# Kernel optimization log

Hardware: AMD Instinct MI355X
Metric: run time of the kernel (lower is better)

Reference implementation:

```python
import jax, jax.numpy as jnp
import numpy as np

N, E, D, G = 50000, 640000, 128, 64
STEPS = 4

def _leaky(z):
    return jnp.where(z >= 0, z, 0.01 * z)

def _lin(x, W, b):
    return x @ W.T + b

def setup_inputs() -> dict:
    key = jax.random.key(0)
    ks = jax.random.split(key, 16)
    s = 0.05
    inp = {
        "x": jax.random.normal(ks[0], (N, D), jnp.float32),
        "x_global": jax.random.normal(ks[1], (G, D), jnp.float32),
        "edge_attr": jax.random.normal(ks[2], (E, 2), jnp.float32),
        # per-step stacked parameters (torch Linear layout [out,in])
        "Wm": jax.random.normal(ks[3], (STEPS, D, D), jnp.float32) * s,
        "bm": jnp.zeros((STEPS, D), jnp.float32),
        "Wa": jax.random.normal(ks[4], (STEPS, D, 2 * D), jnp.float32) * s,
        "ba": jnp.zeros((STEPS, D), jnp.float32),
        "Wgate": jax.random.normal(ks[5], (STEPS, 1, D), jnp.float32) * s,
        "bgate": jnp.zeros((STEPS, 1), jnp.float32),
        "Wfeat": jax.random.normal(ks[6], (STEPS, D, D), jnp.float32) * s,
        "bfeat": jnp.zeros((STEPS, D), jnp.float32),
        "Wt": jax.random.normal(ks[7], (STEPS, D, 2 * D), jnp.float32) * s,
        "bt": jnp.zeros((STEPS, D), jnp.float32),
        "edge_index": jax.random.randint(ks[8], (2, E), 0, N, jnp.int32),
        "batch_ind": jnp.sort(jax.random.randint(ks[9], (N,), 0, G, jnp.int32)),
        "num_graphs": G,
    }
    return inp

def reference(x, x_global, edge_attr, Wm, bm, Wa, ba, Wgate, bgate, Wfeat, bfeat, Wt, bt, edge_index, batch_ind, num_graphs):
    src, dst = edge_index[0], edge_index[1]
    n = x.shape[0]
    for i in range(Wm.shape[0]):
        # GraphNet: gather -> Linear+LeakyReLU -> scatter-max -> concat -> Linear+LeakyReLU + residual
        msg = _leaky(_lin(x[src], Wm[i], bm[i]))                     # [E, agg]
        agg = jax.ops.segment_max(msg, dst, num_segments=n)
        agg = jnp.where(jnp.isfinite(agg), agg, 0.0)                 # PyG fills empty with 0
        x = _leaky(_lin(jnp.concatenate([x, agg], axis=1), Wa[i], ba[i])) + x
        # GlobalNode: attentional aggregation (segment softmax) + transform + residual
        gate = _lin(x, Wgate[i], bgate[i])[:, 0]                     # [N]
        feat = _leaky(_lin(x, Wfeat[i], bfeat[i]))                   # [N, D]
        gmax = jax.ops.segment_max(gate, batch_ind, num_segments=num_graphs)
        gmax = jnp.where(jnp.isfinite(gmax), gmax, 0.0)
        e = jnp.exp(gate - gmax[batch_ind])
        denom = jax.ops.segment_sum(e, batch_ind, num_segments=num_graphs)
        denom = jnp.where(denom == 0, 1.0, denom)
        alpha = e / denom[batch_ind]
        xg = jax.ops.segment_sum(alpha[:, None] * feat, batch_ind, num_segments=num_graphs)
        cat = jnp.concatenate([xg, x_global], axis=1)
        x_global = _leaky(_lin(cat, Wt[i], bt[i])) + x_global
    return (x, x_global)
```

## Files before the change

### kernel.cpp

```cpp
#include <hip/hip_runtime.h>
#include <hip/hip_bf16.h>

#define NN 50000
#define EE 640000
#define DD 128
#define GG 64
#define STEPS 4
#define XP 32
#define NB 196

static inline int cdiv(int a, int b) { return (a + b - 1) / b; }

typedef __attribute__((ext_vector_type(8))) short bf16x8;
typedef __attribute__((ext_vector_type(4))) float f32x4;

__device__ __forceinline__ float lk(float z) { return z >= 0.f ? z : 0.01f * z; }
__device__ __forceinline__ float b2f(short b) { return __uint_as_float(((unsigned)(unsigned short)b) << 16); }
__device__ __forceinline__ unsigned short f2b(float f) {
    unsigned u = __float_as_uint(f);
    return (unsigned short)((u + 0x7FFFu + ((u >> 16) & 1u)) >> 16);
}

__global__ void k_f2b(const float* __restrict__ in, unsigned short* __restrict__ out, int n4) {
    int i = blockIdx.x * blockDim.x + threadIdx.x;
    if (i < n4) {
        float4 v = reinterpret_cast<const float4*>(in)[i];
        ushort4 o;
        o.x = f2b(v.x); o.y = f2b(v.y); o.z = f2b(v.z); o.w = f2b(v.w);
        reinterpret_cast<ushort4*>(out)[i] = o;
    }
}

#define WC1 (STEPS * DD * DD / 4)
#define WC2 (STEPS * DD * 2 * DD / 4)
#define WC3 (STEPS * DD * DD / 4)
__global__ void k_wcvt(const float* __restrict__ Wm, const float* __restrict__ Wa, const float* __restrict__ Wf,
                       unsigned short* __restrict__ Wm_b, unsigned short* __restrict__ Wa_b,
                       unsigned short* __restrict__ Wf_b) {
    int i = blockIdx.x * blockDim.x + threadIdx.x;
    const float* src; unsigned short* dst; int j = i;
    if (j < WC1) { src = Wm; dst = Wm_b; }
    else {
        j -= WC1;
        if (j < WC2) { src = Wa; dst = Wa_b; }
        else {
            j -= WC2;
            if (j >= WC3) return;
            src = Wf; dst = Wf_b;
        }
    }
    float4 v = reinterpret_cast<const float4*>(src)[j];
    ushort4 o;
    o.x = f2b(v.x); o.y = f2b(v.y); o.z = f2b(v.z); o.w = f2b(v.w);
    reinterpret_cast<ushort4*>(dst)[j] = o;
}

__global__ void k_count(const int* __restrict__ dst, int* __restrict__ deg) {
    int e = blockIdx.x * blockDim.x + threadIdx.x;
    if (e < EE) atomicAdd(&deg[dst[e]], 1);
}

__global__ __launch_bounds__(256) void k_scan1(const int* __restrict__ deg, int* __restrict__ off,
                                               int* __restrict__ bsum) {
    __shared__ int ws[4];
    int tid = threadIdx.x, lane = tid & 63, wv = tid >> 6;
    int i = blockIdx.x * 256 + tid;
    int v = (i < NN) ? deg[i] : 0;
    int x = v;
    #pragma unroll
    for (int o = 1; o < 64; o <<= 1) { int t = __shfl_up(x, o); if (lane >= o) x += t; }
    if (lane == 63) ws[wv] = x;
    __syncthreads();
    int wbase = 0;
    #pragma unroll
    for (int p = 0; p < 3; ++p) if (p < wv) wbase += ws[p];
    if (i < NN) off[i] = wbase + x - v;
    if (tid == 255) bsum[blockIdx.x] = wbase + x;
}

__global__ __launch_bounds__(256) void k_scan2(const int* __restrict__ bsum, int* __restrict__ boff,
                                               int* __restrict__ off) {
    __shared__ int ws[4];
    int tid = threadIdx.x, lane = tid & 63, wv = tid >> 6;
    int v = (tid < NB) ? bsum[tid] : 0;
    int x = v;
    #pragma unroll
    for (int o = 1; o < 64; o <<= 1) { int t = __shfl_up(x, o); if (lane >= o) x += t; }
    if (lane == 63) ws[wv] = x;
    __syncthreads();
    int wbase = 0;
    #pragma unroll
    for (int p = 0; p < 3; ++p) if (p < wv) wbase += ws[p];
    if (tid < NB) boff[tid] = wbase + x - v;
    if (tid == 255) off[NN] = wbase + x;
}

__global__ __launch_bounds__(256) void k_scan3(const int* __restrict__ boff, int* __restrict__ off,
                                               int* __restrict__ cursor) {
    int i = blockIdx.x * 256 + threadIdx.x;
    if (i < NN) {
        int o = off[i] + boff[blockIdx.x];
        off[i] = o;
        cursor[i] = o;
    }
}

__global__ void k_fill(const int* __restrict__ src, const int* __restrict__ dst,
                       int* __restrict__ cursor, int* __restrict__ csr) {
    int e = blockIdx.x * blockDim.x + threadIdx.x;
    if (e < EE) {
        int d = dst[e];
        int p = atomicAdd(&cursor[d], 1);
        csr[p] = src[e];
    }
}

__global__ void k_goff(const int* __restrict__ batch, int* __restrict__ goff) {
    int i = blockIdx.x * blockDim.x + threadIdx.x;
    if (i >= NN) return;
    int b = batch[i];
    int prev = (i == 0) ? -1 : batch[i - 1];
    for (int g = prev + 1; g <= b; ++g) goff[g] = i;
    if (i == NN - 1) for (int g = b + 1; g <= GG; ++g) goff[g] = NN;
}

template<int KDIM, bool TWO_IN, bool RESID, bool GATE>
__global__ __launch_bounds__(256) void k_mfma(
    const unsigned short* __restrict__ X1b, const unsigned short* __restrict__ X2b,
    const unsigned short* __restrict__ Wb, const float* __restrict__ bias,
    unsigned short* __restrict__ Yb, float* __restrict__ Yf, const float* __restrict__ resid,
    const float* __restrict__ wgf, const float* __restrict__ bgp, float* __restrict__ gate)
{
    __shared__ float sY[64 * 128];
    const int tid = threadIdx.x;
    const int wv = tid >> 6, lane = tid & 63;
    const int lo = lane & 15, hi = lane >> 4;
    const int n0 = blockIdx.x * 64;
    const int arow = n0 + wv * 16 + lo;
    const bool rvalid = arow < NN;

    f32x4 acc[8];
    #pragma unroll
    for (int t = 0; t < 8; ++t) acc[t] = (f32x4){0.f, 0.f, 0.f, 0.f};

    constexpr int KCH = KDIM / 32;
    #pragma unroll
    for (int kc = 0; kc < KCH; ++kc) {
        const int k = kc * 32 + hi * 8;
        bf16x8 a = (bf16x8)(short)0;
        if (rvalid) {
            if (TWO_IN) {
                const unsigned short* base = (k < 128) ? &X1b[(size_t)arow * 128 + k]
                                                       : &X2b[(size_t)arow * 128 + (k - 128)];
                a = *reinterpret_cast<const bf16x8*>(base);
            } else {
                a = *reinterpret_cast<const bf16x8*>(&X1b[(size_t)arow * KDIM + k]);
            }
        }
        #pragma unroll
        for (int t = 0; t < 8; ++t) {
            const int o = t * 16 + lo;
            bf16x8 b = *reinterpret_cast<const bf16x8*>(&Wb[(size_t)o * KDIM + k]);
            acc[t] = __builtin_amdgcn_mfma_f32_16x16x32_bf16(a, b, acc[t], 0, 0, 0);
        }
    }

    const int lrow = wv * 16 + hi * 4;
    const int swz1 = (hi & 1) << 4;
    #pragma unroll
    for (int t = 0; t < 8; ++t) {
        const int col = (t * 16 + lo) ^ swz1;
        const float bc = bias[t * 16 + lo];
        #pragma unroll
        for (int r = 0; r < 4; ++r)
            sY[(lrow + r) * 128 + col] = lk(acc[t][r] + bc);
    }
    __syncthreads();

    if (RESID) {
        const float bg0 = GATE ? bgp[0] : 0.f;
        #pragma unroll
        for (int it = 0; it < 8; ++it) {
            const int idx = it * 256 + tid;
            const int row = idx >> 5, u4 = (idx & 31) * 4;
            const int n = n0 + row;
            const bool valid = n < NN;
            const int ux = u4 ^ (((row >> 2) & 1) << 4);
            float4 v = *reinterpret_cast<const float4*>(&sY[row * 128 + ux]);
            if (valid) {
                float4 rsd = *reinterpret_cast<const float4*>(&resid[(size_t)n * 128 + u4]);
                v.x += rsd.x; v.y += rsd.y; v.z += rsd.z; v.w += rsd.w;
                *reinterpret_cast<float4*>(&Yf[(size_t)n * 128 + u4]) = v;
                ushort4 ob;
                ob.x = f2b(v.x); ob.y = f2b(v.y); ob.z = f2b(v.z); ob.w = f2b(v.w);
                *reinterpret_cast<ushort4*>(&Yb[(size_t)n * 128 + u4]) = ob;
            }
            if (GATE) {
                float4 wg4 = *reinterpret_cast<const float4*>(&wgf[u4]);
                float gs = valid ? (v.x * wg4.x + v.y * wg4.y + v.z * wg4.z + v.w * wg4.w) : 0.f;
                #pragma unroll
                for (int sh = 16; sh > 0; sh >>= 1) gs += __shfl_xor(gs, sh);
                if ((lane & 31) == 0 && valid) gate[n] = gs + bg0;
            }
        }
    } else {
        #pragma unroll
        for (int it = 0; it < 4; ++it) {
            const int idx = it * 256 + tid;
            const int row = idx >> 4, ub = (idx & 15) * 8;
            const int n = n0 + row;
            if (n < NN) {
                const int ubx = ub ^ (((row >> 2) & 1) << 4);
                bf16x8 ob;
                #pragma unroll
                for (int j = 0; j < 8; ++j) ob[j] = (short)f2b(sY[row * 128 + ubx + j]);
                *reinterpret_cast<bf16x8*>(&Yb[(size_t)n * 128 + ub]) = ob;
            }
        }
    }
}

__global__ __launch_bounds__(256) void k_aggmax(const unsigned short* __restrict__ yb,
                                                const int* __restrict__ off,
                                                const int* __restrict__ csr,
                                                unsigned short* __restrict__ aggb) {
    int gtid = blockIdx.x * blockDim.x + threadIdx.x;
    int node = gtid >> 6;
    if (node >= NN) return;
    int lane = threadIdx.x & 63;
    int slot = lane >> 4, c8 = (lane & 15) * 8;
    int b = off[node], e = off[node + 1];
    int deg = e - b;
    float m[8];
    #pragma unroll
    for (int j = 0; j < 8; ++j) m[j] = -3.4e38f;
    if (deg > 0) {
        int T = (deg + 7) >> 3;
        for (int it = 0; it < T; ++it) {
            int p0 = b + it * 8 + slot;
            int p1 = p0 + 4;
            int i0 = csr[p0 < e ? p0 : b];
            int i1 = csr[p1 < e ? p1 : b];
            bf16x8 v0 = *reinterpret_cast<const bf16x8*>(&yb[(size_t)i0 * 128 + c8]);
            bf16x8 v1 = *reinterpret_cast<const bf16x8*>(&yb[(size_t)i1 * 128 + c8]);
            #pragma unroll
            for (int j = 0; j < 8; ++j) m[j] = fmaxf(m[j], fmaxf(b2f(v0[j]), b2f(v1[j])));
        }
    }
    #pragma unroll
    for (int j = 0; j < 8; ++j) m[j] = fmaxf(m[j], __shfl_xor(m[j], 16));
    #pragma unroll
    for (int j = 0; j < 8; ++j) m[j] = fmaxf(m[j], __shfl_xor(m[j], 32));
    if (slot == 0) {
        bf16x8 o;
        #pragma unroll
        for (int j = 0; j < 8; ++j) o[j] = (deg > 0) ? (short)f2b(m[j]) : (short)0;
        *reinterpret_cast<bf16x8*>(&aggb[(size_t)node * 128 + c8]) = o;
    }
}

__global__ __launch_bounds__(256) void k_gstats(const float* __restrict__ gate, const int* __restrict__ goff,
                                                float* __restrict__ efac, float* __restrict__ invden) {
    __shared__ float red[256];
    int g = blockIdx.x;
    int tid = threadIdx.x;
    int b = goff[g], e = goff[g + 1];
    float m = -3.4e38f;
    for (int i = b + tid; i < e; i += 256) m = fmaxf(m, gate[i]);
    red[tid] = m; __syncthreads();
    for (int o = 128; o > 0; o >>= 1) { if (tid < o) red[tid] = fmaxf(red[tid], red[tid + o]); __syncthreads(); }
    float gm = red[0];
    __syncthreads();
    float s = 0.f;
    for (int i = b + tid; i < e; i += 256) { float ev = __expf(gate[i] - gm); efac[i] = ev; s += ev; }
    red[tid] = s; __syncthreads();
    for (int o = 128; o > 0; o >>= 1) { if (tid < o) red[tid] += red[tid + o]; __syncthreads(); }
    if (tid == 0) { float d = red[0]; if (d == 0.f) d = 1.f; invden[g] = 1.f / d; }
}

__global__ __launch_bounds__(128) void k_xgpart(const float* __restrict__ efac,
                                                const unsigned short* __restrict__ featb,
                                                const int* __restrict__ goff, float* __restrict__ part) {
    int g = blockIdx.x >> 5, p = blockIdx.x & 31;
    int d = threadIdx.x;
    int b = goff[g], e = goff[g + 1];
    int len = e - b;
    int chunk = (len + XP - 1) / XP;
    int s0 = b + p * chunk;
    int s1 = min(e, s0 + chunk);
    float acc = 0.f;
    #pragma unroll 2
    for (int i = s0; i < s1; ++i) acc += efac[i] * b2f(featb[(size_t)i * 128 + d]);
    part[((size_t)g * XP + p) * 128 + d] = acc;
}

__global__ __launch_bounds__(128) void k_gtrans(const float* __restrict__ part, const float* __restrict__ invden,
                                                const float* __restrict__ Wt, const float* __restrict__ bt,
                                                float* __restrict__ xglob) {
    __shared__ float cat[256];
    int g = blockIdx.x;
    int o = threadIdx.x;
    float xgv = 0.f;
    #pragma unroll
    for (int p = 0; p < XP; ++p) xgv += part[((size_t)g * XP + p) * 128 + o];
    cat[o] = xgv * invden[g];
    cat[128 + o] = xglob[(size_t)g * 128 + o];
    __syncthreads();
    float accv = bt[o];
    const float4* w4 = reinterpret_cast<const float4*>(&Wt[(size_t)o * 256]);
    #pragma unroll 8
    for (int k4 = 0; k4 < 64; ++k4) {
        float4 wv = w4[k4];
        accv += cat[4 * k4 + 0] * wv.x + cat[4 * k4 + 1] * wv.y + cat[4 * k4 + 2] * wv.z + cat[4 * k4 + 3] * wv.w;
    }
    float outv = lk(accv) + cat[128 + o];
    xglob[(size_t)g * 128 + o] = outv;
}

extern "C" void kernel_launch(void* const* d_in, const int* in_sizes, int n_in,
                              void* d_out, int out_size, void* d_ws, size_t ws_size,
                              hipStream_t stream) {
    const float* x_in  = (const float*)d_in[0];
    const float* xg_in = (const float*)d_in[1];
    const float* Wm = (const float*)d_in[3];
    const float* bm = (const float*)d_in[4];
    const float* Wa = (const float*)d_in[5];
    const float* ba = (const float*)d_in[6];
    const float* Wg = (const float*)d_in[7];
    const float* bg = (const float*)d_in[8];
    const float* Wf = (const float*)d_in[9];
    const float* bf = (const float*)d_in[10];
    const float* Wt = (const float*)d_in[11];
    const float* bt = (const float*)d_in[12];
    const int* eidx  = (const int*)d_in[13];
    const int* batch = (const int*)d_in[14];

    float* xout  = (float*)d_out;
    float* xglob = xout + (size_t)NN * DD;

    char* w = (char*)d_ws;
    unsigned short* yb   = (unsigned short*)w; w += (size_t)NN * DD * 2;
    unsigned short* aggb = (unsigned short*)w; w += (size_t)NN * DD * 2;
    unsigned short* xb   = (unsigned short*)w; w += (size_t)NN * DD * 2;
    unsigned short* Wm_b = (unsigned short*)w; w += (size_t)STEPS * DD * DD * 2;
    unsigned short* Wa_b = (unsigned short*)w; w += (size_t)STEPS * DD * 2 * DD * 2;
    unsigned short* Wf_b = (unsigned short*)w; w += (size_t)STEPS * DD * DD * 2;
    float* gate   = (float*)w; w += (size_t)NN * 4;
    float* efac   = (float*)w; w += (size_t)NN * 4;
    float* part   = (float*)w; w += (size_t)GG * XP * DD * 4;
    float* invden = (float*)w; w += (size_t)GG * 4;
    int* deg    = (int*)w; w += (size_t)(NN + 1) * 4;
    int* off    = (int*)w; w += (size_t)(NN + 1) * 4;
    int* cursor = (int*)w; w += (size_t)NN * 4;
    int* csr    = (int*)w; w += (size_t)EE * 4;
    int* goff   = (int*)w; w += (size_t)(GG + 1) * 4;
    int* bsum   = (int*)w; w += (size_t)NB * 4;
    int* boff   = (int*)w; w += (size_t)NB * 4;

    const int* srcI = eidx;
    const int* dstI = eidx + EE;

    hipMemcpyAsync(xout,  x_in,  (size_t)NN * DD * 4, hipMemcpyDeviceToDevice, stream);
    hipMemcpyAsync(xglob, xg_in, (size_t)GG * DD * 4, hipMemcpyDeviceToDevice, stream);

    k_f2b<<<cdiv(NN * DD / 4, 256), 256, 0, stream>>>(x_in, xb, NN * DD / 4);
    k_wcvt<<<cdiv(WC1 + WC2 + WC3, 256), 256, 0, stream>>>(Wm, Wa, Wf, Wm_b, Wa_b, Wf_b);

    hipMemsetAsync(deg, 0, (size_t)NN * 4, stream);
    k_count<<<cdiv(EE, 256), 256, 0, stream>>>(dstI, deg);
    k_scan1<<<NB, 256, 0, stream>>>(deg, off, bsum);
    k_scan2<<<1, 256, 0, stream>>>(bsum, boff, off);
    k_scan3<<<NB, 256, 0, stream>>>(boff, off, cursor);
    k_fill<<<cdiv(EE, 256), 256, 0, stream>>>(srcI, dstI, cursor, csr);
    k_goff<<<cdiv(NN, 256), 256, 0, stream>>>(batch, goff);

    const int gemmGrid = cdiv(NN, 64);
    const int aggGrid  = cdiv(NN * 64, 256);

    for (int i = 0; i < STEPS; ++i) {
        const unsigned short* Wmi = Wm_b + (size_t)i * DD * DD;
        const float* bmi = bm + (size_t)i * DD;
        const unsigned short* Wai = Wa_b + (size_t)i * DD * 2 * DD;
        const float* bai = ba + (size_t)i * DD;
        const float* Wgi = Wg + (size_t)i * DD;
        const float* bgi = bg + (size_t)i;
        const unsigned short* Wfi = Wf_b + (size_t)i * DD * DD;
        const float* bfi = bf + (size_t)i * DD;
        const float* Wti = Wt + (size_t)i * DD * 2 * DD;
        const float* bti = bt + (size_t)i * DD;

        k_mfma<128, false, false, false><<<gemmGrid, 256, 0, stream>>>(
            xb, nullptr, Wmi, bmi, yb, nullptr, nullptr, nullptr, nullptr, nullptr);
        k_aggmax<<<aggGrid, 256, 0, stream>>>(yb, off, csr, aggb);
        k_mfma<256, true, true, true><<<gemmGrid, 256, 0, stream>>>(
            xb, aggb, Wai, bai, xb, xout, xout, Wgi, bgi, gate);
        k_mfma<128, false, false, false><<<gemmGrid, 256, 0, stream>>>(
            xb, nullptr, Wfi, bfi, yb, nullptr, nullptr, nullptr, nullptr, nullptr);
        k_gstats<<<GG, 256, 0, stream>>>(gate, goff, efac, invden);
        k_xgpart<<<GG * XP, 128, 0, stream>>>(efac, yb, goff, part);
        k_gtrans<<<GG, 128, 0, stream>>>(part, invden, Wti, bti, xglob);
    }
}
```

Before: 603.1 us.

## Fuse next-step message GEMM with feature GEMM sharing one read of x

```diff
diff --git a/kernel.cpp b/kernel.cpp
--- a/kernel.cpp
+++ b/kernel.cpp
@@ -124,24 +124,27 @@
     if (i == NN - 1) for (int g = b + 1; g <= GG; ++g) goff[g] = NN;
 }
 
-template<int KDIM, bool TWO_IN, bool RESID, bool GATE>
+template<int KDIM, bool TWO_IN, bool RESID, bool GATE, bool OUT2>
 __global__ __launch_bounds__(256) void k_mfma(
     const unsigned short* __restrict__ X1b, const unsigned short* __restrict__ X2b,
-    const unsigned short* __restrict__ Wb, const float* __restrict__ bias,
-    unsigned short* __restrict__ Yb, float* __restrict__ Yf, const float* __restrict__ resid,
+    const unsigned short* __restrict__ W1, const float* __restrict__ b1,
+    const unsigned short* __restrict__ W2, const float* __restrict__ b2,
+    unsigned short* __restrict__ Yb1, unsigned short* __restrict__ Yb2,
+    float* __restrict__ Yf, const float* __restrict__ resid,
     const float* __restrict__ wgf, const float* __restrict__ bgp, float* __restrict__ gate)
 {
-    __shared__ float sY[64 * 128];
+    __shared__ float sY[32 * 128];
     const int tid = threadIdx.x;
     const int wv = tid >> 6, lane = tid & 63;
     const int lo = lane & 15, hi = lane >> 4;
-    const int n0 = blockIdx.x * 64;
-    const int arow = n0 + wv * 16 + lo;
+    const int rw = wv >> 1, cw = wv & 1;
+    const int n0 = blockIdx.x * 32;
+    const int arow = n0 + rw * 16 + lo;
     const bool rvalid = arow < NN;
 
-    f32x4 acc[8];
-    #pragma unroll
-    for (int t = 0; t < 8; ++t) acc[t] = (f32x4){0.f, 0.f, 0.f, 0.f};
+    f32x4 acc1[4], acc2[4];
+    #pragma unroll
+    for (int t = 0; t < 4; ++t) { acc1[t] = (f32x4){0.f,0.f,0.f,0.f}; acc2[t] = (f32x4){0.f,0.f,0.f,0.f}; }
 
     constexpr int KCH = KDIM / 32;
     #pragma unroll
@@ -158,29 +161,34 @@
             }
         }
         #pragma unroll
-        for (int t = 0; t < 8; ++t) {
-            const int o = t * 16 + lo;
-            bf16x8 b = *reinterpret_cast<const bf16x8*>(&Wb[(size_t)o * KDIM + k]);
-            acc[t] = __builtin_amdgcn_mfma_f32_16x16x32_bf16(a, b, acc[t], 0, 0, 0);
-        }
-    }
-
-    const int lrow = wv * 16 + hi * 4;
-    const int swz1 = (hi & 1) << 4;
-    #pragma unroll
-    for (int t = 0; t < 8; ++t) {
-        const int col = (t * 16 + lo) ^ swz1;
-        const float bc = bias[t * 16 + lo];
+        for (int t = 0; t < 4; ++t) {
+            const int o = cw * 64 + t * 16 + lo;
+            bf16x8 bv = *reinterpret_cast<const bf16x8*>(&W1[(size_t)o * KDIM + k]);
+            acc1[t] = __builtin_amdgcn_mfma_f32_16x16x32_bf16(a, bv, acc1[t], 0, 0, 0);
+            if (OUT2) {
+                bf16x8 bv2 = *reinterpret_cast<const bf16x8*>(&W2[(size_t)o * KDIM + k]);
+                acc2[t] = __builtin_amdgcn_mfma_f32_16x16x32_bf16(a, bv2, acc2[t], 0, 0, 0);
+            }
+        }
+    }
+
+    const int lrow = rw * 16 + hi * 4;
+    const int swz = (hi & 1) << 4;
+    #pragma unroll
+    for (int t = 0; t < 4; ++t) {
+        const int oc = cw * 64 + t * 16 + lo;
+        const int col = oc ^ swz;
+        const float bc = b1[oc];
         #pragma unroll
         for (int r = 0; r < 4; ++r)
-            sY[(lrow + r) * 128 + col] = lk(acc[t][r] + bc);
+            sY[(lrow + r) * 128 + col] = lk(acc1[t][r] + bc);
     }
     __syncthreads();
 
     if (RESID) {
         const float bg0 = GATE ? bgp[0] : 0.f;
         #pragma unroll
-        for (int it = 0; it < 8; ++it) {
+        for (int it = 0; it < 4; ++it) {
             const int idx = it * 256 + tid;
             const int row = idx >> 5, u4 = (idx & 31) * 4;
             const int n = n0 + row;
@@ -193,7 +201,7 @@
                 *reinterpret_cast<float4*>(&Yf[(size_t)n * 128 + u4]) = v;
                 ushort4 ob;
                 ob.x = f2b(v.x); ob.y = f2b(v.y); ob.z = f2b(v.z); ob.w = f2b(v.w);
-                *reinterpret_cast<ushort4*>(&Yb[(size_t)n * 128 + u4]) = ob;
+                *reinterpret_cast<ushort4*>(&Yb1[(size_t)n * 128 + u4]) = ob;
             }
             if (GATE) {
                 float4 wg4 = *reinterpret_cast<const float4*>(&wgf[u4]);
@@ -205,7 +213,7 @@
         }
     } else {
         #pragma unroll
-        for (int it = 0; it < 4; ++it) {
+        for (int it = 0; it < 2; ++it) {
             const int idx = it * 256 + tid;
             const int row = idx >> 4, ub = (idx & 15) * 8;
             const int n = n0 + row;
@@ -214,7 +222,34 @@
                 bf16x8 ob;
                 #pragma unroll
                 for (int j = 0; j < 8; ++j) ob[j] = (short)f2b(sY[row * 128 + ubx + j]);
-                *reinterpret_cast<bf16x8*>(&Yb[(size_t)n * 128 + ub]) = ob;
+                *reinterpret_cast<bf16x8*>(&Yb1[(size_t)n * 128 + ub]) = ob;
+            }
+        }
+    }
+
+    if (OUT2) {
+        __syncthreads();
+        #pragma unroll
+        for (int t = 0; t < 4; ++t) {
+            const int oc = cw * 64 + t * 16 + lo;
+            const int col = oc ^ swz;
+            const float bc = b2[oc];
+            #pragma unroll
+            for (int r = 0; r < 4; ++r)
+                sY[(lrow + r) * 128 + col] = lk(acc2[t][r] + bc);
+        }
+        __syncthreads();
+        #pragma unroll
+        for (int it = 0; it < 2; ++it) {
+            const int idx = it * 256 + tid;
+            const int row = idx >> 4, ub = (idx & 15) * 8;
+            const int n = n0 + row;
+            if (n < NN) {
+                const int ubx = ub ^ (((row >> 2) & 1) << 4);
+                bf16x8 ob;
+                #pragma unroll
+                for (int j = 0; j < 8; ++j) ob[j] = (short)f2b(sY[row * 128 + ubx + j]);
+                *reinterpret_cast<bf16x8*>(&Yb2[(size_t)n * 128 + ub]) = ob;
             }
         }
     }
@@ -339,12 +374,13 @@
     float* xglob = xout + (size_t)NN * DD;
 
     char* w = (char*)d_ws;
-    unsigned short* yb   = (unsigned short*)w; w += (size_t)NN * DD * 2;
-    unsigned short* aggb = (unsigned short*)w; w += (size_t)NN * DD * 2;
-    unsigned short* xb   = (unsigned short*)w; w += (size_t)NN * DD * 2;
-    unsigned short* Wm_b = (unsigned short*)w; w += (size_t)STEPS * DD * DD * 2;
-    unsigned short* Wa_b = (unsigned short*)w; w += (size_t)STEPS * DD * 2 * DD * 2;
-    unsigned short* Wf_b = (unsigned short*)w; w += (size_t)STEPS * DD * DD * 2;
+    unsigned short* yb    = (unsigned short*)w; w += (size_t)NN * DD * 2;
+    unsigned short* featb = (unsigned short*)w; w += (size_t)NN * DD * 2;
+    unsigned short* aggb  = (unsigned short*)w; w += (size_t)NN * DD * 2;
+    unsigned short* xb    = (unsigned short*)w; w += (size_t)NN * DD * 2;
+    unsigned short* Wm_b  = (unsigned short*)w; w += (size_t)STEPS * DD * DD * 2;
+    unsigned short* Wa_b  = (unsigned short*)w; w += (size_t)STEPS * DD * 2 * DD * 2;
+    unsigned short* Wf_b  = (unsigned short*)w; w += (size_t)STEPS * DD * DD * 2;
     float* gate   = (float*)w; w += (size_t)NN * 4;
     float* efac   = (float*)w; w += (size_t)NN * 4;
     float* part   = (float*)w; w += (size_t)GG * XP * DD * 4;
@@ -374,14 +410,15 @@
     k_fill<<<cdiv(EE, 256), 256, 0, stream>>>(srcI, dstI, cursor, csr);
     k_goff<<<cdiv(NN, 256), 256, 0, stream>>>(batch, goff);
 
-    const int gemmGrid = cdiv(NN, 64);
+    const int gemmGrid = cdiv(NN, 32);
     const int aggGrid  = cdiv(NN * 64, 256);
 
+    k_mfma<128, false, false, false, false><<<gemmGrid, 256, 0, stream>>>(
+        xb, nullptr, Wm_b, bm, nullptr, nullptr, yb, nullptr, nullptr, nullptr, nullptr, nullptr, nullptr);
+
     for (int i = 0; i < STEPS; ++i) {
-        const unsigned short* Wmi = Wm_b + (size_t)i * DD * DD;
-        const float* bmi = bm + (size_t)i * DD;
+        const float* bai = ba + (size_t)i * DD;
         const unsigned short* Wai = Wa_b + (size_t)i * DD * 2 * DD;
-        const float* bai = ba + (size_t)i * DD;
         const float* Wgi = Wg + (size_t)i * DD;
         const float* bgi = bg + (size_t)i;
         const unsigned short* Wfi = Wf_b + (size_t)i * DD * DD;
@@ -389,15 +426,20 @@
         const float* Wti = Wt + (size_t)i * DD * 2 * DD;
         const float* bti = bt + (size_t)i * DD;
 
-        k_mfma<128, false, false, false><<<gemmGrid, 256, 0, stream>>>(
-            xb, nullptr, Wmi, bmi, yb, nullptr, nullptr, nullptr, nullptr, nullptr);
         k_aggmax<<<aggGrid, 256, 0, stream>>>(yb, off, csr, aggb);
-        k_mfma<256, true, true, true><<<gemmGrid, 256, 0, stream>>>(
-            xb, aggb, Wai, bai, xb, xout, xout, Wgi, bgi, gate);
-        k_mfma<128, false, false, false><<<gemmGrid, 256, 0, stream>>>(
-            xb, nullptr, Wfi, bfi, yb, nullptr, nullptr, nullptr, nullptr, nullptr);
+        k_mfma<256, true, true, true, false><<<gemmGrid, 256, 0, stream>>>(
+            xb, aggb, Wai, bai, nullptr, nullptr, xb, nullptr, xout, xout, Wgi, bgi, gate);
+        if (i < STEPS - 1) {
+            const unsigned short* Wmn = Wm_b + (size_t)(i + 1) * DD * DD;
+            const float* bmn = bm + (size_t)(i + 1) * DD;
+            k_mfma<128, false, false, false, true><<<gemmGrid, 256, 0, stream>>>(
+                xb, nullptr, Wfi, bfi, Wmn, bmn, featb, yb, nullptr, nullptr, nullptr, nullptr, nullptr);
+        } else {
+            k_mfma<128, false, false, false, false><<<gemmGrid, 256, 0, stream>>>(
+                xb, nullptr, Wfi, bfi, nullptr, nullptr, featb, nullptr, nullptr, nullptr, nullptr, nullptr, nullptr);
+        }
         k_gstats<<<GG, 256, 0, stream>>>(gate, goff, efac, invden);
-        k_xgpart<<<GG * XP, 128, 0, stream>>>(efac, yb, goff, part);
+        k_xgpart<<<GG * XP, 128, 0, stream>>>(efac, featb, goff, part);
         k_gtrans<<<GG, 128, 0, stream>>>(part, invden, Wti, bti, xglob);
     }
 }
```

New measurement: 569.3 us. -5.6%, faster.
